# Optimization experiments

Measured on AMD Instinct MI355X. Metric: run time of the kernel, lower is better.

Reference implementation:

```python
import jax, jax.numpy as jnp
import numpy as np

# dims (see shape_source)
N = 20000      # spots / graph nodes
G = 3000       # genes
NF = 256       # NFeature = CrossAttention dim
D_IN = 256     # dims_spot[0]
HID = 64       # dims_spot[1]
OUT = 16       # dims_spot[2]
H = 3          # GATv2 heads
E1 = 640000
E2 = 320000
SLOPE = 0.2    # leaky relu negative slope (GATv2 + CrossAttention alpha)


def _gat_params(key, din, hid, heads):
    k = jax.random.split(key, 3)
    s = 1.0 / np.sqrt(din)
    Wl = jax.random.normal(k[0], (din, heads * hid), jnp.float32) * s
    Wr = jax.random.normal(k[1], (din, heads * hid), jnp.float32) * s
    att = jax.random.normal(k[2], (heads, hid), jnp.float32) * s
    bl = jnp.zeros((heads * hid,), jnp.float32)
    br = jnp.zeros((heads * hid,), jnp.float32)
    b = jnp.zeros((hid,), jnp.float32)
    return Wl, bl, Wr, br, att, b


def setup_inputs() -> dict:
    key = jax.random.key(0)
    ks = jax.random.split(key, 16)
    inp = {
        "gene_freq_mtx": jax.random.normal(ks[0], (NF, G), jnp.float32),
        "gene_eigvecs_T": jax.random.normal(ks[1], (G, N), jnp.float32) / np.sqrt(G),
        "spot_freq_mtx": jax.random.normal(ks[2], (N, D_IN), jnp.float32),
        "spot_eigvecs_T": jax.random.normal(ks[3], (D_IN, NF), jnp.float32) / np.sqrt(D_IN),
        "spotnet": jax.random.randint(ks[4], (2, E1), 0, N, jnp.int32),
        "spotnet_cluster": jax.random.randint(ks[5], (2, E2), 0, N, jnp.int32),
    }
    for name, din, kk in [("c1", D_IN, ks[6]), ("c1p", D_IN, ks[7]), ("c3", OUT, ks[8]), ("c3p", OUT, ks[9])]:
        Wl, bl, Wr, br, att, b = _gat_params(kk, din, HID, H)
        inp[name + "_Wl"] = Wl; inp[name + "_bl"] = bl
        inp[name + "_Wr"] = Wr; inp[name + "_br"] = br
        inp[name + "_att"] = att; inp[name + "_b"] = b
    inp["W2"] = jax.random.normal(ks[10], (2 * HID, OUT), jnp.float32) / np.sqrt(2 * HID)
    inp["b2"] = jnp.zeros((OUT,), jnp.float32)
    inp["W4"] = jax.random.normal(ks[11], (2 * HID, D_IN), jnp.float32) / np.sqrt(2 * HID)
    inp["b4"] = jnp.zeros((D_IN,), jnp.float32)
    inp["a1"] = jax.random.normal(ks[12], (2 * NF, 1), jnp.float32) * 0.05
    inp["a2"] = jax.random.normal(ks[13], (2 * NF, 1), jnp.float32) * 0.05
    return inp


def gatv2(x, edge_index, Wl, bl, Wr, br, att, b, n):
    """PyG GATv2Conv, concat=False (head mean), add_self_loops=False, eval mode."""
    heads, c = att.shape
    src, dst = edge_index[0], edge_index[1]
    xl = (x @ Wl + bl).reshape(-1, heads, c)   # source transform [N,H,C]
    xr = (x @ Wr + br).reshape(-1, heads, c)   # target transform [N,H,C]
    m = jax.nn.leaky_relu(xl[src] + xr[dst], SLOPE)          # [E,H,C]
    e = jnp.einsum('ehc,hc->eh', m, att)                      # [E,H]
    emax = jax.ops.segment_max(e, dst, num_segments=n)        # [N,H]
    emax = jnp.where(jnp.isfinite(emax), emax, 0.0)           # empty segments
    p = jnp.exp(e - emax[dst])
    denom = jax.ops.segment_sum(p, dst, num_segments=n)       # [N,H]
    alpha = p / jnp.maximum(denom, 1e-16)[dst]                # segment softmax
    out = jax.ops.segment_sum(alpha[:, :, None] * xl[src], dst, num_segments=n)
    return out.mean(axis=1) + b                                # [N,C]


def reference(gene_freq_mtx, gene_eigvecs_T, spot_freq_mtx, spot_eigvecs_T,
              c1_Wl, c1_bl, c1_Wr, c1_br, c1_att, c1_b,
              c1p_Wl, c1p_bl, c1p_Wr, c1p_br, c1p_att, c1p_b,
              W2, b2,
              c3_Wl, c3_bl, c3_Wr, c3_br, c3_att, c3_b,
              c3p_Wl, c3p_bl, c3p_Wr, c3p_br, c3p_att, c3p_b,
              W4, b4, a1, a2, spotnet, spotnet_cluster):
    n = spot_freq_mtx.shape[0]
    # GAT (cluster=True)
    h1n = gatv2(spot_freq_mtx, spotnet, c1_Wl, c1_bl, c1_Wr, c1_br, c1_att, c1_b, n)
    h1p = gatv2(spot_freq_mtx, spotnet_cluster, c1p_Wl, c1p_bl, c1p_Wr, c1p_br, c1p_att, c1p_b, n)
    h1 = jax.nn.elu(jnp.concatenate([h1n, h1p], axis=1))
    h2 = h1 @ W2 + b2                                          # emb_spot [N,OUT]
    h3n = gatv2(h2, spotnet, c3_Wl, c3_bl, c3_Wr, c3_br, c3_att, c3_b, n)
    h3p = gatv2(h2, spotnet_cluster, c3p_Wl, c3p_bl, c3p_Wr, c3p_br, c3p_att, c3p_b, n)
    h3 = jax.nn.elu(jnp.concatenate([h3n, h3p], axis=1))
    h4 = h3 @ W4 + b4                                          # mtx_res_spot [N,D_IN]
    # iGFT + clip-at-zero (== relu)
    Xg = jax.nn.relu(gene_eigvecs_T.T @ gene_freq_mtx.T)       # [N,NF]
    Xs = jax.nn.relu(h4 @ spot_eigvecs_T)                      # [N,NF]
    # CrossAttention (dropout=0.0)
    cat = jnp.concatenate([Xg, Xs], axis=1)                    # [N,2NF]
    e = jax.nn.leaky_relu(jnp.concatenate([cat @ a1, cat @ a2], axis=1), SLOPE)
    lam = jax.nn.softmax(e, axis=1)                            # [N,2]
    res = lam[:, :1] * Xg + lam[:, 1:] * Xs
    return (res, lam, h2, h4)
```

## Files before the change

kernel.cpp:

```cpp
#include <hip/hip_runtime.h>

typedef unsigned short u16;
typedef __attribute__((ext_vector_type(8))) short bf16x8;
typedef __attribute__((ext_vector_type(4))) float floatx4;

#define NSPOT 20000
#define NGENE 3000
#define E1N   640000
#define E2N   320000

#define OFF_RES 0
#define OFF_LAM 5120000
#define OFF_H2  5160000
#define OFF_H4  5480000

__device__ __forceinline__ float b2f(u16 u){
  union { unsigned int i; float f; } v; v.i = ((unsigned int)u) << 16; return v.f;
}
__device__ __forceinline__ u16 f2b(float f){
  union { float f; unsigned int i; } v; v.f = f;
  unsigned int i = v.i;
  return (u16)((i + 0x7FFFu + ((i >> 16) & 1u)) >> 16);
}
__device__ __forceinline__ void stout(void* O, size_t i, float v, int isbf){
  if (isbf) ((u16*)O)[i] = f2b(v); else ((float*)O)[i] = v;
}
__device__ __forceinline__ u16 ldu(const void* p, size_t i, int isbf){
  return isbf ? ((const u16*)p)[i] : f2b(((const float*)p)[i]);
}

__global__ void sniff_kernel(const u16* __restrict__ x, int* __restrict__ flag){
  int lane = threadIdx.x;
  u16 u = x[lane * 2];
  int e = (u >> 7) & 0xFF;
  int sane = (u == 0) || (e >= 0x60 && e <= 0xA0);
  unsigned long long b = __ballot(sane);
  if (lane == 0) flag[0] = (__popcll(b) >= 48) ? 1 : 0;
}

struct ConvSeg { const void* src; u16* dst; int n; };
struct ConvBatch { ConvSeg s[14]; };
__global__ void convbatch_kernel(ConvBatch cb, const int* __restrict__ dflag){
  ConvSeg S = cb.s[blockIdx.y];
  int i = blockIdx.x * 256 + threadIdx.x;
  if (i < S.n) S.dst[i] = ldu(S.src, i, dflag[0]);
}

__global__ void conv4_kernel(const void* __restrict__ src, u16* __restrict__ dst, int n4,
                             const int* __restrict__ dflag){
  int i = blockIdx.x * 256 + threadIdx.x;
  if (i >= n4) return;
  size_t b = (size_t)i * 4;
  u16 o[4];
  if (dflag[0]){
    *(uint2*)o = *(const uint2*)((const u16*)src + b);
  } else {
    float4 f = *(const float4*)((const float*)src + b);
    o[0]=f2b(f.x); o[1]=f2b(f.y); o[2]=f2b(f.z); o[3]=f2b(f.w);
  }
  *(uint2*)(dst + b) = *(uint2*)o;
}

__global__ __launch_bounds__(256) void transpose_kernel(
    const void* __restrict__ GE, u16* __restrict__ AT,
    const int* __restrict__ dflag, int K, int M){
  __shared__ float tile[64 * 65];
  int isbf = dflag[0];
  int m0 = blockIdx.x * 64, k0 = blockIdx.y * 64;
#pragma unroll
  for (int i = 0; i < 4; i++){
    int idx = threadIdx.x + i * 256;
    int kr = idx >> 4, mc = (idx & 15) * 4;
    int gk = k0 + kr, gm = m0 + mc;
    if (gk < K){
      float v0 = 0.f, v1 = 0.f, v2 = 0.f, v3 = 0.f;
      if (gm + 4 <= M){
        if (isbf){
          const u16* pp = (const u16*)GE + (size_t)gk * M + gm;
          v0 = b2f(pp[0]); v1 = b2f(pp[1]); v2 = b2f(pp[2]); v3 = b2f(pp[3]);
        } else {
          float4 f = *(const float4*)((const float*)GE + (size_t)gk * M + gm);
          v0 = f.x; v1 = f.y; v2 = f.z; v3 = f.w;
        }
      } else {
        for (int e = 0; e < 4; e++){
          if (gm + e < M){
            float t = isbf ? b2f(((const u16*)GE)[(size_t)gk * M + gm + e])
                           : ((const float*)GE)[(size_t)gk * M + gm + e];
            if (e == 0) v0 = t; else if (e == 1) v1 = t; else if (e == 2) v2 = t; else v3 = t;
          }
        }
      }
      tile[(mc + 0) * 65 + kr] = v0;
      tile[(mc + 1) * 65 + kr] = v1;
      tile[(mc + 2) * 65 + kr] = v2;
      tile[(mc + 3) * 65 + kr] = v3;
    }
  }
  __syncthreads();
#pragma unroll
  for (int i = 0; i < 2; i++){
    int idx = threadIdx.x + i * 256;
    int mr = idx >> 3, kc = (idx & 7) * 8;
    int gm = m0 + mr, gk = k0 + kc;
    if (gm < M && gk < K){
      if (gk + 8 <= K){
        u16 o[8];
#pragma unroll
        for (int e = 0; e < 8; e++) o[e] = f2b(tile[mr * 65 + kc + e]);
        *(uint4*)&AT[(size_t)gm * K + gk] = *(uint4*)o;
      } else {
        for (int e = 0; e < 8 && gk + e < K; e++)
          AT[(size_t)gm * K + gk + e] = f2b(tile[mr * 65 + kc + e]);
      }
    }
  }
}

__global__ void hist_kernel(const int* __restrict__ dst, int* __restrict__ cnt, int E){
  int e = blockIdx.x * 256 + threadIdx.x;
  if (e < E){ int d = dst[e]; if ((unsigned)d < (unsigned)NSPOT) atomicAdd(&cnt[d], 1); }
}

__global__ void scan_kernel(const int* __restrict__ cnt, int* __restrict__ off,
                            int* __restrict__ cur, int n){
  __shared__ int part[256];
  int tid = threadIdx.x;
  int chunk = (n + 255) / 256;
  int lo = tid * chunk; if (lo > n) lo = n;
  int hi = lo + chunk; if (hi > n) hi = n;
  int s = 0;
  for (int i = lo; i < hi; i++) s += cnt[i];
  part[tid] = s;
  __syncthreads();
  if (tid == 0){
    int run = 0;
    for (int i = 0; i < 256; i++){ int t = part[i]; part[i] = run; run += t; }
  }
  __syncthreads();
  int run = part[tid];
  for (int i = lo; i < hi; i++){ off[i] = run; cur[i] = run; run += cnt[i]; }
  if (hi == n) off[n] = run;
}

__global__ void scatter_kernel(const int* __restrict__ src, const int* __restrict__ dst,
                               int* __restrict__ cur, int* __restrict__ out, int E){
  int e = blockIdx.x * 256 + threadIdx.x;
  if (e < E){
    int d = dst[e];
    if ((unsigned)d < (unsigned)NSPOT){
      int p = atomicAdd(&cur[d], 1);
      if ((unsigned)p < (unsigned)E) out[p] = src[e];
    }
  }
}

__global__ void assemble_kernel(const void* Wl, const void* bl, const void* Wr, const void* br,
                                const void* Wlp, const void* blp, const void* Wrp, const void* brp,
                                u16* __restrict__ Wcat, u16* __restrict__ bcat, int Kdim,
                                const int* __restrict__ dflag){
  int isbf = dflag[0];
  int idx = blockIdx.x * 256 + threadIdx.x;
  int total = Kdim * 768;
  if (idx < total){
    int k = idx / 768, j = idx % 768;
    int seg = j / 192, jj = j % 192;
    const void* W = (seg == 0) ? Wl : (seg == 1) ? Wr : (seg == 2) ? Wlp : Wrp;
    Wcat[idx] = ldu(W, (size_t)k * 192 + jj, isbf);
  }
  if (idx < 768){
    int seg = idx / 192, jj = idx % 192;
    const void* b = (seg == 0) ? bl : (seg == 1) ? br : (seg == 2) ? blp : brp;
    bcat[idx] = ldu(b, jj, isbf);
  }
}

template<int BMI, bool A_KM, bool B_NK, bool A_EXT, bool B_EXT, bool RELU, bool HAS_BIAS, bool C_OUT>
__global__ __launch_bounds__(256) void gemm_mfma(
    const void* __restrict__ A, const void* __restrict__ B,
    const u16* __restrict__ bias, void* __restrict__ Cp,
    const int* __restrict__ dflag, size_t aoff, size_t coff,
    int M, int N, int K, int lda, int ldb, int ldc)
{
  const int isbf = dflag[0];
  constexpr int BM = 64 * BMI, BK = 32, LDA = BK + 8, LDB = BK + 8;
  __shared__ __align__(16) u16 As[BM * LDA];
  __shared__ __align__(16) u16 Bs[64 * LDB];
  const u16*   A16 = (const u16*)A + aoff;
  const float* A32 = (const float*)A + aoff;
  const u16*   B16 = (const u16*)B;
  const float* B32 = (const float*)B;
  auto ldA = [&](size_t i) -> u16 { return (!A_EXT || isbf) ? A16[i] : f2b(A32[i]); };
  auto ldB = [&](size_t i) -> u16 { return (!B_EXT || isbf) ? B16[i] : f2b(B32[i]); };

  int tid = threadIdx.x;
  int lane = tid & 63, w = tid >> 6;
  int m0 = blockIdx.y * BM, n0 = blockIdx.x * 64;
  floatx4 acc[BMI][4] = {};
  int quad = lane >> 4;
  int nk = (K + BK - 1) / BK;
  for (int kt = 0; kt < nk; kt++){
    int k0 = kt * BK;
    if (!A_KM){
#pragma unroll
      for (int i = 0; i < BMI; i++){
        int id = tid + i * 256;
        int r = id >> 2, c = (id & 3) * 8;
        int gm = m0 + r, gk = k0 + c;
        if (gm < M && gk + 8 <= K){
          if (!A_EXT || isbf){
            *(uint4*)&As[r * LDA + c] = *(const uint4*)(A16 + (size_t)gm * lda + gk);
          } else {
            const float* p = A32 + (size_t)gm * lda + gk;
            float4 f0 = *(const float4*)p, f1 = *(const float4*)(p + 4);
            u16* d = &As[r * LDA + c];
            d[0]=f2b(f0.x); d[1]=f2b(f0.y); d[2]=f2b(f0.z); d[3]=f2b(f0.w);
            d[4]=f2b(f1.x); d[5]=f2b(f1.y); d[6]=f2b(f1.z); d[7]=f2b(f1.w);
          }
        } else {
          for (int e = 0; e < 8; e++)
            As[r * LDA + c + e] = (gm < M && gk + e < K) ? ldA((size_t)gm * lda + gk + e) : (u16)0;
        }
      }
    } else {
#pragma unroll
      for (int i = 0; i < BMI; i++){
        int id = tid + i * 256;
        int kk, rr;
        if (BMI == 2){ kk = id >> 4; rr = (id & 15) * 8; }
        else         { kk = id >> 3; rr = (id & 7) * 8; }
        int gk = k0 + kk, gm = m0 + rr;
        if (gk < K && gm + 8 <= M){
          if (!A_EXT || isbf){
            uint4 v = *(const uint4*)(A16 + (size_t)gk * lda + gm);
            const u16* pv = (const u16*)&v;
#pragma unroll
            for (int e = 0; e < 8; e++) As[(rr + e) * LDA + kk] = pv[e];
          } else {
            const float* p = A32 + (size_t)gk * lda + gm;
            float4 f0 = *(const float4*)p, f1 = *(const float4*)(p + 4);
            As[(rr+0)*LDA+kk]=f2b(f0.x); As[(rr+1)*LDA+kk]=f2b(f0.y);
            As[(rr+2)*LDA+kk]=f2b(f0.z); As[(rr+3)*LDA+kk]=f2b(f0.w);
            As[(rr+4)*LDA+kk]=f2b(f1.x); As[(rr+5)*LDA+kk]=f2b(f1.y);
            As[(rr+6)*LDA+kk]=f2b(f1.z); As[(rr+7)*LDA+kk]=f2b(f1.w);
          }
        } else {
          for (int e = 0; e < 8; e++)
            As[(rr + e) * LDA + kk] = (gk < K && gm + e < M) ? ldA((size_t)gk * lda + gm + e) : (u16)0;
        }
      }
    }
    if (B_NK){
      int r = tid >> 2, c = (tid & 3) * 8;
      int gn = n0 + r, gk = k0 + c;
      if (gn < N && gk + 8 <= K){
        if (!B_EXT || isbf){
          *(uint4*)&Bs[r * LDB + c] = *(const uint4*)(B16 + (size_t)gn * ldb + gk);
        } else {
          const float* p = B32 + (size_t)gn * ldb + gk;
          float4 f0 = *(const float4*)p, f1 = *(const float4*)(p + 4);
          u16* d = &Bs[r * LDB + c];
          d[0]=f2b(f0.x); d[1]=f2b(f0.y); d[2]=f2b(f0.z); d[3]=f2b(f0.w);
          d[4]=f2b(f1.x); d[5]=f2b(f1.y); d[6]=f2b(f1.z); d[7]=f2b(f1.w);
        }
      } else {
        for (int e = 0; e < 8; e++)
          Bs[r * LDB + c + e] = (gn < N && gk + e < K) ? ldB((size_t)gn * ldb + gk + e) : (u16)0;
      }
    } else {
      int kk = tid >> 3, nn = (tid & 7) * 8;
      int gk = k0 + kk, gn = n0 + nn;
      if (gk < K && gn + 8 <= N){
        if (!B_EXT || isbf){
          uint4 v = *(const uint4*)(B16 + (size_t)gk * ldb + gn);
          const u16* pv = (const u16*)&v;
#pragma unroll
          for (int e = 0; e < 8; e++) Bs[(nn + e) * LDB + kk] = pv[e];
        } else {
          const float* p = B32 + (size_t)gk * ldb + gn;
          float4 f0 = *(const float4*)p, f1 = *(const float4*)(p + 4);
          Bs[(nn+0)*LDB+kk]=f2b(f0.x); Bs[(nn+1)*LDB+kk]=f2b(f0.y);
          Bs[(nn+2)*LDB+kk]=f2b(f0.z); Bs[(nn+3)*LDB+kk]=f2b(f0.w);
          Bs[(nn+4)*LDB+kk]=f2b(f1.x); Bs[(nn+5)*LDB+kk]=f2b(f1.y);
          Bs[(nn+6)*LDB+kk]=f2b(f1.z); Bs[(nn+7)*LDB+kk]=f2b(f1.w);
        }
      } else {
        for (int e = 0; e < 8; e++)
          Bs[(nn + e) * LDB + kk] = (gk < K && gn + e < N) ? ldB((size_t)gk * ldb + gn + e) : (u16)0;
      }
    }
    __syncthreads();
    bf16x8 af[BMI];
#pragma unroll
    for (int mi = 0; mi < BMI; mi++)
      af[mi] = *(const bf16x8*)&As[(w * (16 * BMI) + mi * 16 + (lane & 15)) * LDA + quad * 8];
#pragma unroll
    for (int ni = 0; ni < 4; ni++){
      bf16x8 bfr = *(const bf16x8*)&Bs[(ni * 16 + (lane & 15)) * LDB + quad * 8];
#pragma unroll
      for (int mi = 0; mi < BMI; mi++)
        acc[mi][ni] = __builtin_amdgcn_mfma_f32_16x16x32_bf16(af[mi], bfr, acc[mi][ni], 0, 0, 0);
    }
    __syncthreads();
  }
#pragma unroll
  for (int mi = 0; mi < BMI; mi++)
#pragma unroll
    for (int ni = 0; ni < 4; ni++)
#pragma unroll
      for (int r = 0; r < 4; r++){
        int row = m0 + w * (16 * BMI) + mi * 16 + quad * 4 + r;
        int col = n0 + ni * 16 + (lane & 15);
        if (row < M && col < N){
          float v = acc[mi][ni][r];
          if (HAS_BIAS) v += b2f(bias[col]);
          if (RELU) v = fmaxf(v, 0.f);
          size_t ci = coff + (size_t)row * ldc + col;
          if (!C_OUT) ((u16*)Cp)[ci] = f2b(v);
          else stout(Cp, ci, v, isbf);
        }
      }
}

__global__ __launch_bounds__(256) void gat_kernel(
    const u16* __restrict__ Y, int xl_off, int xr_off,
    const int* __restrict__ off, const int* __restrict__ srcs,
    const u16* __restrict__ att, const u16* __restrict__ bias,
    u16* __restrict__ aggout, int out_off, int n, int E)
{
  int wid = (blockIdx.x * 256 + threadIdx.x) >> 6;
  int lane = threadIdx.x & 63;
  if (wid >= n) return;
  int sub = lane >> 4;
  int cbase = (lane & 15) * 4;
  const int ldY = 768;
  size_t drow = (size_t)wid * ldY;

  float xr[3][4], at[3][4];
#pragma unroll
  for (int h = 0; h < 3; h++){
    uint2 vx = *(const uint2*)(Y + drow + xr_off + h * 64 + cbase);
    uint2 va = *(const uint2*)(att + h * 64 + cbase);
    const u16* px = (const u16*)&vx;
    const u16* pa = (const u16*)&va;
#pragma unroll
    for (int j = 0; j < 4; j++){ xr[h][j] = b2f(px[j]); at[h][j] = b2f(pa[j]); }
  }

  int beg = off[wid], end = off[wid + 1];
  beg = max(0, min(beg, E));
  end = max(beg, min(end, E));

  float mh[3] = {-INFINITY, -INFINITY, -INFINITY};
  float lh[3] = {0.f, 0.f, 0.f};
  float ac[3][4] = {};

  uint2 xa[3] = {};
  int s_b = 0;
  if (beg < end){
    int e0 = beg + sub;
    int s = (e0 < end) ? srcs[e0] : 0;
    if ((unsigned)s >= (unsigned)NSPOT) s = 0;
    const u16* p = Y + (size_t)s * ldY + xl_off + cbase;
#pragma unroll
    for (int h = 0; h < 3; h++) xa[h] = *(const uint2*)(p + h * 64);
    if (beg + 4 < end){
      int e1 = beg + 4 + sub;
      int s1 = (e1 < end) ? srcs[e1] : 0;
      if ((unsigned)s1 >= (unsigned)NSPOT) s1 = 0;
      s_b = s1;
    }
  }

  for (int b = beg; b < end; b += 4){
    uint2 xc[3];
#pragma unroll
    for (int h = 0; h < 3; h++) xc[h] = xa[h];
    bool act = (b + sub) < end;

    if (b + 4 < end){
      const u16* p = Y + (size_t)s_b * ldY + xl_off + cbase;
#pragma unroll
      for (int h = 0; h < 3; h++) xa[h] = *(const uint2*)(p + h * 64);
      if (b + 8 < end){
        int e2 = b + 8 + sub;
        int s2 = (e2 < end) ? srcs[e2] : 0;
        if ((unsigned)s2 >= (unsigned)NSPOT) s2 = 0;
        s_b = s2;
      }
    }

    float xl[3][4];
    float t0, t1, t2;
    {
      float a0 = 0.f, a1 = 0.f, a2 = 0.f;
      const u16* p0 = (const u16*)&xc[0];
      const u16* p1 = (const u16*)&xc[1];
      const u16* p2 = (const u16*)&xc[2];
#pragma unroll
      for (int j = 0; j < 4; j++){
        float x0 = b2f(p0[j]); xl[0][j] = x0;
        float u0 = x0 + xr[0][j]; u0 = fmaxf(u0, 0.2f * u0);
        a0 = __builtin_fmaf(at[0][j], u0, a0);
        float x1 = b2f(p1[j]); xl[1][j] = x1;
        float u1 = x1 + xr[1][j]; u1 = fmaxf(u1, 0.2f * u1);
        a1 = __builtin_fmaf(at[1][j], u1, a1);
        float x2 = b2f(p2[j]); xl[2][j] = x2;
        float u2 = x2 + xr[2][j]; u2 = fmaxf(u2, 0.2f * u2);
        a2 = __builtin_fmaf(at[2][j], u2, a2);
      }
      t0 = a0; t1 = a1; t2 = a2;
    }
#pragma unroll
    for (int d = 1; d < 16; d <<= 1){
      t0 += __shfl_xor(t0, d, 64);
      t1 += __shfl_xor(t1, d, 64);
      t2 += __shfl_xor(t2, d, 64);
    }
    if (act){
      float tt[3] = {t0, t1, t2};
#pragma unroll
      for (int h = 0; h < 3; h++){
        float nm = fmaxf(mh[h], tt[h]);
        if (nm > mh[h]){
          float sc = __expf(mh[h] - nm);
          lh[h] *= sc;
#pragma unroll
          for (int j = 0; j < 4; j++) ac[h][j] *= sc;
          mh[h] = nm;
        }
        float w = __expf(tt[h] - mh[h]);
        lh[h] += w;
#pragma unroll
        for (int j = 0; j < 4; j++) ac[h][j] = __builtin_fmaf(w, xl[h][j], ac[h][j]);
      }
    }
  }

  float o[4] = {0.f, 0.f, 0.f, 0.f};
#pragma unroll
  for (int h = 0; h < 3; h++){
    float gm = fmaxf(mh[h], __shfl_xor(mh[h], 16, 64));
    gm = fmaxf(gm, __shfl_xor(gm, 32, 64));
    float sc = (mh[h] == -INFINITY) ? 0.f : __expf(mh[h] - gm);
    float L = lh[h] * sc;
    L += __shfl_xor(L, 16, 64);
    L += __shfl_xor(L, 32, 64);
    float inv = 1.f / fmaxf(L, 1e-16f);
#pragma unroll
    for (int j = 0; j < 4; j++){
      float a = ac[h][j] * sc;
      a += __shfl_xor(a, 16, 64);
      a += __shfl_xor(a, 32, 64);
      o[j] += a * inv;
    }
  }
  if (sub == 0){
    u16 ov[4];
#pragma unroll
    for (int j = 0; j < 4; j++){
      float v = o[j] * (1.f / 3.f) + b2f(bias[cbase + j]);
      v = (v > 0.f) ? v : expm1f(v);
      if (!(fabsf(v) < 1e30f)) v = 0.f;
      ov[j] = f2b(v);
    }
    *(uint2*)&aggout[(size_t)wid * 128 + out_off + cbase] = *(uint2*)ov;
  }
}

__global__ __launch_bounds__(256) void h2_kernel(const u16* __restrict__ AGG,
                                                 const u16* __restrict__ W2, const u16* __restrict__ b2,
                                                 float* __restrict__ H2, void* __restrict__ OUT,
                                                 const int* __restrict__ dflag, int n){
  __shared__ float w2s[128 * 16];
  __shared__ float as_[16][128];
  int isbf = dflag[0];
  int tid = threadIdx.x;
  for (int i = tid; i < 128 * 16; i += 256) w2s[i] = b2f(W2[i]);
  int m0 = blockIdx.x * 16;
  for (int i = tid; i < 16 * 128; i += 256){
    int r = i >> 7, c = i & 127; int m = m0 + r;
    as_[r][c] = (m < n) ? b2f(AGG[(size_t)m * 128 + c]) : 0.f;
  }
  __syncthreads();
  int r = tid >> 4, j = tid & 15;
  int m = m0 + r;
  float acc = b2f(b2[j]);
  for (int k = 0; k < 128; k++) acc += as_[r][k] * w2s[k * 16 + j];
  if (m < n){
    H2[(size_t)m * 16 + j] = acc;
    stout(OUT, (size_t)OFF_H2 + (size_t)m * 16 + j, acc, isbf);
  }
}

__global__ __launch_bounds__(256) void y2_kernel(const float* __restrict__ H2,
                                                 const u16* __restrict__ Wcat2, const u16* __restrict__ bcat2,
                                                 u16* __restrict__ Y2, int n){
  __shared__ u16 ws_[16 * 768];
  __shared__ float h[16][16];
  int tid = threadIdx.x;
  for (int i = tid; i < 16 * 768; i += 256) ws_[i] = Wcat2[i];
  int m0 = blockIdx.x * 16;
  {
    int r = tid >> 4, k = tid & 15; int m = m0 + r;
    h[r][k] = (m < n) ? H2[(size_t)m * 16 + k] : 0.f;
  }
  __syncthreads();
  int j = tid;
  float acc[16][3];
  float bj0 = b2f(bcat2[j]), bj1 = b2f(bcat2[j + 256]), bj2 = b2f(bcat2[j + 512]);
#pragma unroll
  for (int r = 0; r < 16; r++){ acc[r][0] = bj0; acc[r][1] = bj1; acc[r][2] = bj2; }
  for (int k = 0; k < 16; k++){
    float w0 = b2f(ws_[k * 768 + j]);
    float w1 = b2f(ws_[k * 768 + j + 256]);
    float w2 = b2f(ws_[k * 768 + j + 512]);
#pragma unroll
    for (int r = 0; r < 16; r++){
      float hv = h[r][k];
      acc[r][0] += hv * w0; acc[r][1] += hv * w1; acc[r][2] += hv * w2;
    }
  }
#pragma unroll
  for (int r = 0; r < 16; r++){
    int m = m0 + r;
    if (m < n){
      size_t base = (size_t)m * 768;
      Y2[base + j] = f2b(acc[r][0]);
      Y2[base + j + 256] = f2b(acc[r][1]);
      Y2[base + j + 512] = f2b(acc[r][2]);
    }
  }
}

__global__ __launch_bounds__(256) void cross_attn_kernel(
    const u16* __restrict__ XG, const u16* __restrict__ XS,
    const u16* __restrict__ a1, const u16* __restrict__ a2,
    void* __restrict__ OUT, const int* __restrict__ dflag, int n){
  int wid = (blockIdx.x * 256 + threadIdx.x) >> 6;
  int lane = threadIdx.x & 63;
  if (wid >= n) return;
  int isbf = dflag[0];
  int c0 = lane * 4;
  size_t base = (size_t)wid * 256 + c0;
  float g[4], s[4];
#pragma unroll
  for (int e = 0; e < 4; e++){ g[e] = b2f(XG[base + e]); s[e] = b2f(XS[base + e]); }
  float p1 = 0.f, p2 = 0.f;
#pragma unroll
  for (int e = 0; e < 4; e++){
    p1 += g[e] * b2f(a1[c0 + e]) + s[e] * b2f(a1[256 + c0 + e]);
    p2 += g[e] * b2f(a2[c0 + e]) + s[e] * b2f(a2[256 + c0 + e]);
  }
#pragma unroll
  for (int d = 32; d > 0; d >>= 1){
    p1 += __shfl_xor(p1, d, 64);
    p2 += __shfl_xor(p2, d, 64);
  }
  float e1 = (p1 > 0.f) ? p1 : 0.2f * p1;
  float e2 = (p2 > 0.f) ? p2 : 0.2f * p2;
  float mx = fmaxf(e1, e2);
  float w1 = __expf(e1 - mx), w2 = __expf(e2 - mx);
  float inv = 1.f / (w1 + w2);
  float l0 = w1 * inv, l1 = w2 * inv;
#pragma unroll
  for (int e = 0; e < 4; e++)
    stout(OUT, (size_t)OFF_RES + base + e, l0 * g[e] + l1 * s[e], isbf);
  if (lane == 0){
    stout(OUT, (size_t)OFF_LAM + (size_t)wid * 2,     l0, isbf);
    stout(OUT, (size_t)OFF_LAM + (size_t)wid * 2 + 1, l1, isbf);
  }
}

extern "C" void kernel_launch(void* const* d_in, const int* in_sizes, int n_in,
                              void* d_out, int out_size, void* d_ws, size_t ws_size,
                              hipStream_t stream) {
  const void* gene_freq = d_in[0];
  const void* gene_eig  = d_in[1];
  const void* spot_freq = d_in[2];
  const void* spot_eig  = d_in[3];
  const int* net1 = (const int*)d_in[4];
  const int* net2 = (const int*)d_in[5];
  const void *c1_Wl=d_in[6],  *c1_bl=d_in[7],  *c1_Wr=d_in[8],  *c1_br=d_in[9],  *c1_att=d_in[10], *c1_b=d_in[11];
  const void *c1p_Wl=d_in[12],*c1p_bl=d_in[13],*c1p_Wr=d_in[14],*c1p_br=d_in[15],*c1p_att=d_in[16],*c1p_b=d_in[17];
  const void *c3_Wl=d_in[18], *c3_bl=d_in[19], *c3_Wr=d_in[20], *c3_br=d_in[21], *c3_att=d_in[22], *c3_b=d_in[23];
  const void *c3p_Wl=d_in[24],*c3p_bl=d_in[25],*c3p_Wr=d_in[26],*c3p_br=d_in[27],*c3p_att=d_in[28],*c3p_b=d_in[29];
  const void *W2=d_in[30], *b2=d_in[31], *W4=d_in[32], *b4=d_in[33], *a1=d_in[34], *a2=d_in[35];

  char* p0 = (char*)d_ws;
  char* p = p0;
  auto carve = [&](size_t bytes) -> char* {
    char* r = p; p += (bytes + 255) & ~(size_t)255; return r;
  };
  int*   flag  = (int*) carve(256);
  int*   cnt1  = (int*) carve((NSPOT + 2) * 4);
  int*   off1  = (int*) carve((NSPOT + 2) * 4);
  int*   cur1  = (int*) carve((NSPOT + 2) * 4);
  int*   srcs1 = (int*) carve((size_t)E1N * 4);
  int*   cnt2  = (int*) carve((NSPOT + 2) * 4);
  int*   off2  = (int*) carve((NSPOT + 2) * 4);
  int*   cur2  = (int*) carve((NSPOT + 2) * 4);
  int*   srcs2 = (int*) carve((size_t)E2N * 4);
  u16*   Wcat1 = (u16*) carve(256 * 768 * 2);
  u16*   bcat1 = (u16*) carve(2048);
  u16*   Wcat2 = (u16*) carve(16 * 768 * 2);
  u16*   bcat2 = (u16*) carve(2048);
  u16*   attc1  = (u16*)carve(192 * 2);
  u16*   attc1p = (u16*)carve(192 * 2);
  u16*   attc3  = (u16*)carve(192 * 2);
  u16*   attc3p = (u16*)carve(192 * 2);
  u16*   bc1  = (u16*)carve(64 * 2);
  u16*   bc1p = (u16*)carve(64 * 2);
  u16*   bc3  = (u16*)carve(64 * 2);
  u16*   bc3p = (u16*)carve(64 * 2);
  u16*   W2c  = (u16*)carve(2048 * 2);
  u16*   b2c  = (u16*)carve(16 * 2);
  u16*   W4c  = (u16*)carve(32768 * 2);
  u16*   b4c  = (u16*)carve(256 * 2);
  u16*   a1c  = (u16*)carve(512 * 2);
  u16*   a2c  = (u16*)carve(512 * 2);
  u16*   GF16 = (u16*) carve((size_t)256 * 3000 * 2);
  u16*   SE16 = (u16*) carve((size_t)256 * 256 * 2);
  float* H2   = (float*)carve((size_t)NSPOT * 16 * 4);
  u16*   AGG  = (u16*)  carve((size_t)NSPOT * 128 * 2);
  u16*   XGp  = (u16*)  carve((size_t)NSPOT * 256 * 2);
  char*  R    = carve(0);
  size_t used_common = (size_t)(R - p0);
  size_t needA = used_common + (size_t)NSPOT * NGENE * 2 + 4096;
  bool planA = (ws_size >= needA);

  sniff_kernel<<<1, 64, 0, stream>>>((const u16*)spot_freq, flag);
  hipMemsetAsync(cnt1, 0, NSPOT * 4, stream);
  hipMemsetAsync(cnt2, 0, NSPOT * 4, stream);
  hist_kernel<<<(E1N + 255) / 256, 256, 0, stream>>>(net1 + E1N, cnt1, E1N);
  hist_kernel<<<(E2N + 255) / 256, 256, 0, stream>>>(net2 + E2N, cnt2, E2N);
  scan_kernel<<<1, 256, 0, stream>>>(cnt1, off1, cur1, NSPOT);
  scan_kernel<<<1, 256, 0, stream>>>(cnt2, off2, cur2, NSPOT);
  scatter_kernel<<<(E1N + 255) / 256, 256, 0, stream>>>(net1, net1 + E1N, cur1, srcs1, E1N);
  scatter_kernel<<<(E2N + 255) / 256, 256, 0, stream>>>(net2, net2 + E2N, cur2, srcs2, E2N);

  ConvBatch cb;
  cb.s[0]  = {c1_att,  attc1,  192}; cb.s[1]  = {c1p_att, attc1p, 192};
  cb.s[2]  = {c3_att,  attc3,  192}; cb.s[3]  = {c3p_att, attc3p, 192};
  cb.s[4]  = {c1_b, bc1, 64}; cb.s[5]  = {c1p_b, bc1p, 64};
  cb.s[6]  = {c3_b, bc3, 64}; cb.s[7]  = {c3p_b, bc3p, 64};
  cb.s[8]  = {W2, W2c, 2048}; cb.s[9]  = {b2, b2c, 16};
  cb.s[10] = {W4, W4c, 32768}; cb.s[11] = {b4, b4c, 256};
  cb.s[12] = {a1, a1c, 512}; cb.s[13] = {a2, a2c, 512};
  convbatch_kernel<<<dim3(128, 14), 256, 0, stream>>>(cb, flag);
  conv4_kernel<<<(256 * 3000 / 4 + 255) / 256, 256, 0, stream>>>(gene_freq, GF16, 256 * 3000 / 4, flag);
  conv4_kernel<<<(256 * 256 / 4 + 255) / 256, 256, 0, stream>>>(spot_eig, SE16, 256 * 256 / 4, flag);

  assemble_kernel<<<(256 * 768 + 255) / 256, 256, 0, stream>>>(
      c1_Wl, c1_bl, c1_Wr, c1_br, c1p_Wl, c1p_bl, c1p_Wr, c1p_br, Wcat1, bcat1, 256, flag);
  assemble_kernel<<<(16 * 768 + 255) / 256, 256, 0, stream>>>(
      c3_Wl, c3_bl, c3_Wr, c3_br, c3p_Wl, c3p_bl, c3p_Wr, c3p_br, Wcat2, bcat2, 16, flag);

  if (planA){
    u16* AT   = (u16*)R;
    u16* SF16 = (u16*)R;
    u16* Y    = (u16*)(R + 10485760);
    u16* XS   = (u16*)(R + 10485760 + 31457280);
    u16* XG   = XGp;

    transpose_kernel<<<dim3(313, 47), 256, 0, stream>>>(gene_eig, AT, flag, NGENE, NSPOT);
    gemm_mfma<1, false, true, false, false, true, false, false><<<dim3(4, 313), 256, 0, stream>>>(
        AT, GF16, nullptr, XG, flag, 0, 0, NSPOT, 256, NGENE, NGENE, NGENE, 256);
    conv4_kernel<<<(NSPOT * 256 / 4 + 255) / 256, 256, 0, stream>>>(spot_freq, SF16, NSPOT * 256 / 4, flag);
    gemm_mfma<2, false, false, false, false, false, true, false><<<dim3(12, 157), 256, 0, stream>>>(
        SF16, Wcat1, bcat1, Y, flag, 0, 0, NSPOT, 768, 256, 256, 768, 768);
    gat_kernel<<<5000, 256, 0, stream>>>(Y, 0,   192, off1, srcs1, attc1,  bc1,  AGG, 0,  NSPOT, E1N);
    gat_kernel<<<5000, 256, 0, stream>>>(Y, 384, 576, off2, srcs2, attc1p, bc1p, AGG, 64, NSPOT, E2N);
    h2_kernel<<<1250, 256, 0, stream>>>(AGG, W2c, b2c, H2, d_out, flag, NSPOT);
    y2_kernel<<<1250, 256, 0, stream>>>(H2, Wcat2, bcat2, Y, NSPOT);
    gat_kernel<<<5000, 256, 0, stream>>>(Y, 0,   192, off1, srcs1, attc3,  bc3,  AGG, 0,  NSPOT, E1N);
    gat_kernel<<<5000, 256, 0, stream>>>(Y, 384, 576, off2, srcs2, attc3p, bc3p, AGG, 64, NSPOT, E2N);
    gemm_mfma<1, false, false, false, false, false, true, true><<<dim3(4, 313), 256, 0, stream>>>(
        AGG, W4c, b4c, d_out, flag, 0, OFF_H4, NSPOT, 256, 128, 128, 256, 256);
    gemm_mfma<1, false, false, true, false, true, false, false><<<dim3(4, 313), 256, 0, stream>>>(
        d_out, SE16, nullptr, XS, flag, OFF_H4, 0, NSPOT, 256, 256, 256, 256, 256);
    cross_attn_kernel<<<5000, 256, 0, stream>>>(XG, XS, a1c, a2c, d_out, flag, NSPOT);
  } else {
    u16* Y  = (u16*)R;
    u16* XG = Y;
    u16* XS = Y + 5120000;
    gemm_mfma<2, false, false, true, false, false, true, false><<<dim3(12, 157), 256, 0, stream>>>(
        spot_freq, Wcat1, bcat1, Y, flag, 0, 0, NSPOT, 768, 256, 256, 768, 768);
    gat_kernel<<<5000, 256, 0, stream>>>(Y, 0,   192, off1, srcs1, attc1,  bc1,  AGG, 0,  NSPOT, E1N);
    gat_kernel<<<5000, 256, 0, stream>>>(Y, 384, 576, off2, srcs2, attc1p, bc1p, AGG, 64, NSPOT, E2N);
    h2_kernel<<<1250, 256, 0, stream>>>(AGG, W2c, b2c, H2, d_out, flag, NSPOT);
    y2_kernel<<<1250, 256, 0, stream>>>(H2, Wcat2, bcat2, Y, NSPOT);
    gat_kernel<<<5000, 256, 0, stream>>>(Y, 0,   192, off1, srcs1, attc3,  bc3,  AGG, 0,  NSPOT, E1N);
    gat_kernel<<<5000, 256, 0, stream>>>(Y, 384, 576, off2, srcs2, attc3p, bc3p, AGG, 64, NSPOT, E2N);
    gemm_mfma<2, false, false, false, false, false, true, true><<<dim3(4, 157), 256, 0, stream>>>(
        AGG, W4c, b4c, d_out, flag, 0, OFF_H4, NSPOT, 256, 128, 128, 256, 256);
    gemm_mfma<2, false, false, true, true, true, false, false><<<dim3(4, 157), 256, 0, stream>>>(
        d_out, spot_eig, nullptr, XS, flag, OFF_H4, 0, NSPOT, 256, 256, 256, 256, 256);
    gemm_mfma<2, true, true, true, true, true, false, false><<<dim3(4, 157), 256, 0, stream>>>(
        gene_eig, gene_freq, nullptr, XG, flag, 0, 0, NSPOT, 256, NGENE, NSPOT, NGENE, 256);
    cross_attn_kernel<<<5000, 256, 0, stream>>>(XG, XS, a1c, a2c, d_out, flag, NSPOT);
  }

  (void)in_sizes; (void)n_in; (void)out_size; (void)ws_size;
}
```

Measured before the change: 1.122 ms.

## Batch paired launches, fuse h2/y2, add bf16 h4 side output, enlarge GEMM tiles

After: 1.091 ms. 1.03x faster.

```diff
diff --git a/kernel.cpp b/kernel.cpp
--- a/kernel.cpp
+++ b/kernel.cpp
@@ -46,11 +46,17 @@
   if (i < S.n) S.dst[i] = ldu(S.src, i, dflag[0]);
 }
 
-__global__ void conv4_kernel(const void* __restrict__ src, u16* __restrict__ dst, int n4,
+__global__ void conv3_kernel(const void* __restrict__ s0, u16* __restrict__ d0, int n0,
+                             const void* __restrict__ s1, u16* __restrict__ d1, int n1,
+                             const void* __restrict__ s2, u16* __restrict__ d2, int n2,
                              const int* __restrict__ dflag){
   int i = blockIdx.x * 256 + threadIdx.x;
-  if (i >= n4) return;
-  size_t b = (size_t)i * 4;
+  const void* src; u16* dst; int local;
+  if (i < n0){ src = s0; dst = d0; local = i; }
+  else if (i < n0 + n1){ src = s1; dst = d1; local = i - n0; }
+  else if (i < n0 + n1 + n2){ src = s2; dst = d2; local = i - n0 - n1; }
+  else return;
+  size_t b = (size_t)local * 4;
   u16 o[4];
   if (dflag[0]){
     *(uint2*)o = *(const uint2*)((const u16*)src + b);
@@ -117,13 +123,21 @@
   }
 }
 
-__global__ void hist_kernel(const int* __restrict__ dst, int* __restrict__ cnt, int E){
+__global__ void hist2_kernel(const int* __restrict__ dst0, int E0, int* __restrict__ cnt0,
+                             const int* __restrict__ dst1, int E1, int* __restrict__ cnt1){
+  const int* dst = blockIdx.y ? dst1 : dst0;
+  int* cnt = blockIdx.y ? cnt1 : cnt0;
+  int E = blockIdx.y ? E1 : E0;
   int e = blockIdx.x * 256 + threadIdx.x;
   if (e < E){ int d = dst[e]; if ((unsigned)d < (unsigned)NSPOT) atomicAdd(&cnt[d], 1); }
 }
 
-__global__ void scan_kernel(const int* __restrict__ cnt, int* __restrict__ off,
-                            int* __restrict__ cur, int n){
+__global__ void scan2_kernel(const int* __restrict__ c0, int* __restrict__ o0, int* __restrict__ u0,
+                             const int* __restrict__ c1, int* __restrict__ o1, int* __restrict__ u1,
+                             int n){
+  const int* cnt = blockIdx.x ? c1 : c0;
+  int* off = blockIdx.x ? o1 : o0;
+  int* cur = blockIdx.x ? u1 : u0;
   __shared__ int part[256];
   int tid = threadIdx.x;
   int chunk = (n + 255) / 256;
@@ -143,8 +157,15 @@
   if (hi == n) off[n] = run;
 }
 
-__global__ void scatter_kernel(const int* __restrict__ src, const int* __restrict__ dst,
-                               int* __restrict__ cur, int* __restrict__ out, int E){
+__global__ void scatter2_kernel(const int* __restrict__ src0, const int* __restrict__ dst0,
+                                int* __restrict__ cur0, int* __restrict__ out0, int E0,
+                                const int* __restrict__ src1, const int* __restrict__ dst1,
+                                int* __restrict__ cur1, int* __restrict__ out1, int E1){
+  const int* src = blockIdx.y ? src1 : src0;
+  const int* dst = blockIdx.y ? dst1 : dst0;
+  int* cur = blockIdx.y ? cur1 : cur0;
+  int* out = blockIdx.y ? out1 : out0;
+  int E = blockIdx.y ? E1 : E0;
   int e = blockIdx.x * 256 + threadIdx.x;
   if (e < E){
     int d = dst[e];
@@ -155,32 +176,34 @@
   }
 }
 
-__global__ void assemble_kernel(const void* Wl, const void* bl, const void* Wr, const void* br,
-                                const void* Wlp, const void* blp, const void* Wrp, const void* brp,
-                                u16* __restrict__ Wcat, u16* __restrict__ bcat, int Kdim,
-                                const int* __restrict__ dflag){
+struct AsmSet {
+  const void *Wl, *bl, *Wr, *br, *Wlp, *blp, *Wrp, *brp;
+  u16* Wcat; u16* bcat; int Kdim;
+};
+__global__ void assemble2_kernel(AsmSet s0, AsmSet s1, const int* __restrict__ dflag){
+  AsmSet S = blockIdx.y ? s1 : s0;
   int isbf = dflag[0];
   int idx = blockIdx.x * 256 + threadIdx.x;
-  int total = Kdim * 768;
+  int total = S.Kdim * 768;
   if (idx < total){
     int k = idx / 768, j = idx % 768;
     int seg = j / 192, jj = j % 192;
-    const void* W = (seg == 0) ? Wl : (seg == 1) ? Wr : (seg == 2) ? Wlp : Wrp;
-    Wcat[idx] = ldu(W, (size_t)k * 192 + jj, isbf);
+    const void* W = (seg == 0) ? S.Wl : (seg == 1) ? S.Wr : (seg == 2) ? S.Wlp : S.Wrp;
+    S.Wcat[idx] = ldu(W, (size_t)k * 192 + jj, isbf);
   }
   if (idx < 768){
     int seg = idx / 192, jj = idx % 192;
-    const void* b = (seg == 0) ? bl : (seg == 1) ? br : (seg == 2) ? blp : brp;
-    bcat[idx] = ldu(b, jj, isbf);
-  }
-}
-
-template<int BMI, bool A_KM, bool B_NK, bool A_EXT, bool B_EXT, bool RELU, bool HAS_BIAS, bool C_OUT>
+    const void* b = (seg == 0) ? S.bl : (seg == 1) ? S.br : (seg == 2) ? S.blp : S.brp;
+    S.bcat[idx] = ldu(b, jj, isbf);
+  }
+}
+
+template<int BMI, bool A_KM, bool B_NK, bool A_EXT, bool B_EXT, bool RELU, bool HAS_BIAS, bool C_OUT, bool C2>
 __global__ __launch_bounds__(256) void gemm_mfma(
     const void* __restrict__ A, const void* __restrict__ B,
-    const u16* __restrict__ bias, void* __restrict__ Cp,
+    const u16* __restrict__ bias, void* __restrict__ Cp, u16* __restrict__ Cp2,
     const int* __restrict__ dflag, size_t aoff, size_t coff,
-    int M, int N, int K, int lda, int ldb, int ldc)
+    int M, int N, int K, int lda, int ldb, int ldc, int ldc2)
 {
   const int isbf = dflag[0];
   constexpr int BM = 64 * BMI, BK = 32, LDA = BK + 8, LDB = BK + 8;
@@ -318,17 +341,24 @@
           size_t ci = coff + (size_t)row * ldc + col;
           if (!C_OUT) ((u16*)Cp)[ci] = f2b(v);
           else stout(Cp, ci, v, isbf);
+          if (C2) Cp2[(size_t)row * ldc2 + col] = f2b(v);
         }
       }
 }
 
-__global__ __launch_bounds__(256) void gat_kernel(
-    const u16* __restrict__ Y, int xl_off, int xr_off,
-    const int* __restrict__ off, const int* __restrict__ srcs,
-    const u16* __restrict__ att, const u16* __restrict__ bias,
-    u16* __restrict__ aggout, int out_off, int n, int E)
+struct GatSet {
+  const int* off; const int* srcs; const u16* att; const u16* bias;
+  int xl_off, xr_off, out_off, E;
+};
+__global__ __launch_bounds__(256) void gat2_kernel(
+    const u16* __restrict__ Y, GatSet SA, GatSet SB,
+    u16* __restrict__ aggout, int n)
 {
-  int wid = (blockIdx.x * 256 + threadIdx.x) >> 6;
+  int half = gridDim.x >> 1;
+  int selB = (int)blockIdx.x >= half;
+  GatSet S = selB ? SB : SA;
+  int bx = blockIdx.x - (selB ? half : 0);
+  int wid = (bx * 256 + threadIdx.x) >> 6;
   int lane = threadIdx.x & 63;
   if (wid >= n) return;
   int sub = lane >> 4;
@@ -339,17 +369,17 @@
   float xr[3][4], at[3][4];
 #pragma unroll
   for (int h = 0; h < 3; h++){
-    uint2 vx = *(const uint2*)(Y + drow + xr_off + h * 64 + cbase);
-    uint2 va = *(const uint2*)(att + h * 64 + cbase);
+    uint2 vx = *(const uint2*)(Y + drow + S.xr_off + h * 64 + cbase);
+    uint2 va = *(const uint2*)(S.att + h * 64 + cbase);
     const u16* px = (const u16*)&vx;
     const u16* pa = (const u16*)&va;
 #pragma unroll
     for (int j = 0; j < 4; j++){ xr[h][j] = b2f(px[j]); at[h][j] = b2f(pa[j]); }
   }
 
-  int beg = off[wid], end = off[wid + 1];
-  beg = max(0, min(beg, E));
-  end = max(beg, min(end, E));
+  int beg = S.off[wid], end = S.off[wid + 1];
+  beg = max(0, min(beg, S.E));
+  end = max(beg, min(end, S.E));
 
   float mh[3] = {-INFINITY, -INFINITY, -INFINITY};
   float lh[3] = {0.f, 0.f, 0.f};
@@ -359,14 +389,14 @@
   int s_b = 0;
   if (beg < end){
     int e0 = beg + sub;
-    int s = (e0 < end) ? srcs[e0] : 0;
+    int s = (e0 < end) ? S.srcs[e0] : 0;
     if ((unsigned)s >= (unsigned)NSPOT) s = 0;
-    const u16* p = Y + (size_t)s * ldY + xl_off + cbase;
+    const u16* p = Y + (size_t)s * ldY + S.xl_off + cbase;
 #pragma unroll
     for (int h = 0; h < 3; h++) xa[h] = *(const uint2*)(p + h * 64);
     if (beg + 4 < end){
       int e1 = beg + 4 + sub;
-      int s1 = (e1 < end) ? srcs[e1] : 0;
+      int s1 = (e1 < end) ? S.srcs[e1] : 0;
       if ((unsigned)s1 >= (unsigned)NSPOT) s1 = 0;
       s_b = s1;
     }
@@ -379,12 +409,12 @@
     bool act = (b + sub) < end;
 
     if (b + 4 < end){
-      const u16* p = Y + (size_t)s_b * ldY + xl_off + cbase;
+      const u16* p = Y + (size_t)s_b * ldY + S.xl_off + cbase;
 #pragma unroll
       for (int h = 0; h < 3; h++) xa[h] = *(const uint2*)(p + h * 64);
       if (b + 8 < end){
         int e2 = b + 8 + sub;
-        int s2 = (e2 < end) ? srcs[e2] : 0;
+        int s2 = (e2 < end) ? S.srcs[e2] : 0;
         if ((unsigned)s2 >= (unsigned)NSPOT) s2 = 0;
         s_b = s2;
       }
@@ -459,51 +489,41 @@
     u16 ov[4];
 #pragma unroll
     for (int j = 0; j < 4; j++){
-      float v = o[j] * (1.f / 3.f) + b2f(bias[cbase + j]);
+      float v = o[j] * (1.f / 3.f) + b2f(S.bias[cbase + j]);
       v = (v > 0.f) ? v : expm1f(v);
       if (!(fabsf(v) < 1e30f)) v = 0.f;
       ov[j] = f2b(v);
     }
-    *(uint2*)&aggout[(size_t)wid * 128 + out_off + cbase] = *(uint2*)ov;
-  }
-}
-
-__global__ __launch_bounds__(256) void h2_kernel(const u16* __restrict__ AGG,
-                                                 const u16* __restrict__ W2, const u16* __restrict__ b2,
-                                                 float* __restrict__ H2, void* __restrict__ OUT,
-                                                 const int* __restrict__ dflag, int n){
+    *(uint2*)&aggout[(size_t)wid * 128 + S.out_off + cbase] = *(uint2*)ov;
+  }
+}
+
+__global__ __launch_bounds__(256) void h2y2_kernel(
+    const u16* __restrict__ AGG, const u16* __restrict__ W2, const u16* __restrict__ b2,
+    const u16* __restrict__ Wcat2, const u16* __restrict__ bcat2,
+    void* __restrict__ OUT, u16* __restrict__ Y2,
+    const int* __restrict__ dflag, int n){
   __shared__ float w2s[128 * 16];
   __shared__ float as_[16][128];
+  __shared__ float h[16][16];
+  __shared__ __align__(16) u16 ws_[16 * 768];
   int isbf = dflag[0];
   int tid = threadIdx.x;
   for (int i = tid; i < 128 * 16; i += 256) w2s[i] = b2f(W2[i]);
+  for (int i = tid; i < 1536; i += 256) ((uint4*)ws_)[i] = ((const uint4*)Wcat2)[i];
   int m0 = blockIdx.x * 16;
   for (int i = tid; i < 16 * 128; i += 256){
     int r = i >> 7, c = i & 127; int m = m0 + r;
     as_[r][c] = (m < n) ? b2f(AGG[(size_t)m * 128 + c]) : 0.f;
   }
   __syncthreads();
-  int r = tid >> 4, j = tid & 15;
-  int m = m0 + r;
-  float acc = b2f(b2[j]);
-  for (int k = 0; k < 128; k++) acc += as_[r][k] * w2s[k * 16 + j];
-  if (m < n){
-    H2[(size_t)m * 16 + j] = acc;
-    stout(OUT, (size_t)OFF_H2 + (size_t)m * 16 + j, acc, isbf);
-  }
-}
-
-__global__ __launch_bounds__(256) void y2_kernel(const float* __restrict__ H2,
-                                                 const u16* __restrict__ Wcat2, const u16* __restrict__ bcat2,
-                                                 u16* __restrict__ Y2, int n){
-  __shared__ u16 ws_[16 * 768];
-  __shared__ float h[16][16];
-  int tid = threadIdx.x;
-  for (int i = tid; i < 16 * 768; i += 256) ws_[i] = Wcat2[i];
-  int m0 = blockIdx.x * 16;
   {
-    int r = tid >> 4, k = tid & 15; int m = m0 + r;
-    h[r][k] = (m < n) ? H2[(size_t)m * 16 + k] : 0.f;
+    int r = tid >> 4, j = tid & 15;
+    int m = m0 + r;
+    float acc = b2f(b2[j]);
+    for (int k = 0; k < 128; k++) acc += as_[r][k] * w2s[k * 16 + j];
+    h[r][j] = acc;
+    if (m < n) stout(OUT, (size_t)OFF_H2 + (size_t)m * 16 + j, acc, isbf);
   }
   __syncthreads();
   int j = tid;
@@ -621,23 +641,26 @@
   u16*   a2c  = (u16*)carve(512 * 2);
   u16*   GF16 = (u16*) carve((size_t)256 * 3000 * 2);
   u16*   SE16 = (u16*) carve((size_t)256 * 256 * 2);
-  float* H2   = (float*)carve((size_t)NSPOT * 16 * 4);
-  u16*   AGG  = (u16*)  carve((size_t)NSPOT * 128 * 2);
-  u16*   XGp  = (u16*)  carve((size_t)NSPOT * 256 * 2);
+  u16*   SF16 = (u16*) carve((size_t)NSPOT * 256 * 2);
+  u16*   H4B  = (u16*) carve((size_t)NSPOT * 256 * 2);
+  u16*   AGG  = (u16*) carve((size_t)NSPOT * 128 * 2);
+  u16*   XGp  = (u16*) carve((size_t)NSPOT * 256 * 2);
   char*  R    = carve(0);
   size_t used_common = (size_t)(R - p0);
-  size_t needA = used_common + (size_t)NSPOT * NGENE * 2 + 4096;
+  size_t needA = used_common + (size_t)NSPOT * NGENE * 2
+               + (size_t)NSPOT * 768 * 2
+               + (size_t)NSPOT * 256 * 2
+               + 4096;
   bool planA = (ws_size >= needA);
 
   sniff_kernel<<<1, 64, 0, stream>>>((const u16*)spot_freq, flag);
   hipMemsetAsync(cnt1, 0, NSPOT * 4, stream);
   hipMemsetAsync(cnt2, 0, NSPOT * 4, stream);
-  hist_kernel<<<(E1N + 255) / 256, 256, 0, stream>>>(net1 + E1N, cnt1, E1N);
-  hist_kernel<<<(E2N + 255) / 256, 256, 0, stream>>>(net2 + E2N, cnt2, E2N);
-  scan_kernel<<<1, 256, 0, stream>>>(cnt1, off1, cur1, NSPOT);
-  scan_kernel<<<1, 256, 0, stream>>>(cnt2, off2, cur2, NSPOT);
-  scatter_kernel<<<(E1N + 255) / 256, 256, 0, stream>>>(net1, net1 + E1N, cur1, srcs1, E1N);
-  scatter_kernel<<<(E2N + 255) / 256, 256, 0, stream>>>(net2, net2 + E2N, cur2, srcs2, E2N);
+  hist2_kernel<<<dim3((E1N + 255) / 256, 2), 256, 0, stream>>>(
+      net1 + E1N, E1N, cnt1, net2 + E2N, E2N, cnt2);
+  scan2_kernel<<<2, 256, 0, stream>>>(cnt1, off1, cur1, cnt2, off2, cur2, NSPOT);
+  scatter2_kernel<<<dim3((E1N + 255) / 256, 2), 256, 0, stream>>>(
+      net1, net1 + E1N, cur1, srcs1, E1N, net2, net2 + E2N, cur2, srcs2, E2N);
 
   ConvBatch cb;
   cb.s[0]  = {c1_att,  attc1,  192}; cb.s[1]  = {c1p_att, attc1p, 192};
@@ -648,58 +671,51 @@
   cb.s[10] = {W4, W4c, 32768}; cb.s[11] = {b4, b4c, 256};
   cb.s[12] = {a1, a1c, 512}; cb.s[13] = {a2, a2c, 512};
   convbatch_kernel<<<dim3(128, 14), 256, 0, stream>>>(cb, flag);
-  conv4_kernel<<<(256 * 3000 / 4 + 255) / 256, 256, 0, stream>>>(gene_freq, GF16, 256 * 3000 / 4, flag);
-  conv4_kernel<<<(256 * 256 / 4 + 255) / 256, 256, 0, stream>>>(spot_eig, SE16, 256 * 256 / 4, flag);
-
-  assemble_kernel<<<(256 * 768 + 255) / 256, 256, 0, stream>>>(
-      c1_Wl, c1_bl, c1_Wr, c1_br, c1p_Wl, c1p_bl, c1p_Wr, c1p_br, Wcat1, bcat1, 256, flag);
-  assemble_kernel<<<(16 * 768 + 255) / 256, 256, 0, stream>>>(
-      c3_Wl, c3_bl, c3_Wr, c3_br, c3p_Wl, c3p_bl, c3p_Wr, c3p_br, Wcat2, bcat2, 16, flag);
-
+
+  {
+    int n0 = 256 * 3000 / 4, n1 = 256 * 256 / 4, n2 = NSPOT * 256 / 4;
+    int tot = n0 + n1 + n2;
+    conv3_kernel<<<(tot + 255) / 256, 256, 0, stream>>>(
+        gene_freq, GF16, n0, spot_eig, SE16, n1, spot_freq, SF16, n2, flag);
+  }
+
+  AsmSet as0 = {c1_Wl, c1_bl, c1_Wr, c1_br, c1p_Wl, c1p_bl, c1p_Wr, c1p_br, Wcat1, bcat1, 256};
+  AsmSet as1 = {c3_Wl, c3_bl, c3_Wr, c3_br, c3p_Wl, c3p_bl, c3p_Wr, c3p_br, Wcat2, bcat2, 16};
+  assemble2_kernel<<<dim3((256 * 768 + 255) / 256, 2), 256, 0, stream>>>(as0, as1, flag);
+
+  GatSet g1a = {off1, srcs1, attc1,  bc1,  0,   192, 0,  E1N};
+  GatSet g1b = {off2, srcs2, attc1p, bc1p, 384, 576, 64, E2N};
+  GatSet g3a = {off1, srcs1, attc3,  bc3,  0,   192, 0,  E1N};
+  GatSet g3b = {off2, srcs2, attc3p, bc3p, 384, 576, 64, E2N};
+
+  u16* Y;
+  u16* XS;
+  u16* XG = XGp;
   if (planA){
-    u16* AT   = (u16*)R;
-    u16* SF16 = (u16*)R;
-    u16* Y    = (u16*)(R + 10485760);
-    u16* XS   = (u16*)(R + 10485760 + 31457280);
-    u16* XG   = XGp;
+    u16* AT = (u16*)R;
+    Y  = (u16*)(R + (size_t)NSPOT * NGENE * 2);
+    XS = Y + (size_t)NSPOT * 768;
 
     transpose_kernel<<<dim3(313, 47), 256, 0, stream>>>(gene_eig, AT, flag, NGENE, NSPOT);
-    gemm_mfma<1, false, true, false, false, true, false, false><<<dim3(4, 313), 256, 0, stream>>>(
-        AT, GF16, nullptr, XG, flag, 0, 0, NSPOT, 256, NGENE, NGENE, NGENE, 256);
-    conv4_kernel<<<(NSPOT * 256 / 4 + 255) / 256, 256, 0, stream>>>(spot_freq, SF16, NSPOT * 256 / 4, flag);
-    gemm_mfma<2, false, false, false, false, false, true, false><<<dim3(12, 157), 256, 0, stream>>>(
-        SF16, Wcat1, bcat1, Y, flag, 0, 0, NSPOT, 768, 256, 256, 768, 768);
-    gat_kernel<<<5000, 256, 0, stream>>>(Y, 0,   192, off1, srcs1, attc1,  bc1,  AGG, 0,  NSPOT, E1N);
-    gat_kernel<<<5000, 256, 0, stream>>>(Y, 384, 576, off2, srcs2, attc1p, bc1p, AGG, 64, NSPOT, E2N);
-    h2_kernel<<<1250, 256, 0, stream>>>(AGG, W2c, b2c, H2, d_out, flag, NSPOT);
-    y2_kernel<<<1250, 256, 0, stream>>>(H2, Wcat2, bcat2, Y, NSPOT);
-    gat_kernel<<<5000, 256, 0, stream>>>(Y, 0,   192, off1, srcs1, attc3,  bc3,  AGG, 0,  NSPOT, E1N);
-    gat_kernel<<<5000, 256, 0, stream>>>(Y, 384, 576, off2, srcs2, attc3p, bc3p, AGG, 64, NSPOT, E2N);
-    gemm_mfma<1, false, false, false, false, false, true, true><<<dim3(4, 313), 256, 0, stream>>>(
-        AGG, W4c, b4c, d_out, flag, 0, OFF_H4, NSPOT, 256, 128, 128, 256, 256);
-    gemm_mfma<1, false, false, true, false, true, false, false><<<dim3(4, 313), 256, 0, stream>>>(
-        d_out, SE16, nullptr, XS, flag, OFF_H4, 0, NSPOT, 256, 256, 256, 256, 256);
-    cross_attn_kernel<<<5000, 256, 0, stream>>>(XG, XS, a1c, a2c, d_out, flag, NSPOT);
+    gemm_mfma<2, false, true, false, false, true, false, false, false><<<dim3(4, 157), 256, 0, stream>>>(
+        AT, GF16, nullptr, XG, nullptr, flag, 0, 0, NSPOT, 256, NGENE, NGENE, NGENE, 256, 0);
   } else {
-    u16* Y  = (u16*)R;
-    u16* XG = Y;
-    u16* XS = Y + 5120000;
-    gemm_mfma<2, false, false, true, false, false, true, false><<<dim3(12, 157), 256, 0, stream>>>(
-        spot_freq, Wcat1, bcat1, Y, flag, 0, 0, NSPOT, 768, 256, 256, 768, 768);
-    gat_kernel<<<5000, 256, 0, stream>>>(Y, 0,   192, off1, srcs1, attc1,  bc1,  AGG, 0,  NSPOT, E1N);
-    gat_kernel<<<5000, 256, 0, stream>>>(Y, 384, 576, off2, srcs2, attc1p, bc1p, AGG, 64, NSPOT, E2N);
-    h2_kernel<<<1250, 256, 0, stream>>>(AGG, W2c, b2c, H2, d_out, flag, NSPOT);
-    y2_kernel<<<1250, 256, 0, stream>>>(H2, Wcat2, bcat2, Y, NSPOT);
-    gat_kernel<<<5000, 256, 0, stream>>>(Y, 0,   192, off1, srcs1, attc3,  bc3,  AGG, 0,  NSPOT, E1N);
-    gat_kernel<<<5000, 256, 0, stream>>>(Y, 384, 576, off2, srcs2, attc3p, bc3p, AGG, 64, NSPOT, E2N);
-    gemm_mfma<2, false, false, false, false, false, true, true><<<dim3(4, 157), 256, 0, stream>>>(
-        AGG, W4c, b4c, d_out, flag, 0, OFF_H4, NSPOT, 256, 128, 128, 256, 256);
-    gemm_mfma<2, false, false, true, true, true, false, false><<<dim3(4, 157), 256, 0, stream>>>(
-        d_out, spot_eig, nullptr, XS, flag, OFF_H4, 0, NSPOT, 256, 256, 256, 256, 256);
-    gemm_mfma<2, true, true, true, true, true, false, false><<<dim3(4, 157), 256, 0, stream>>>(
-        gene_eig, gene_freq, nullptr, XG, flag, 0, 0, NSPOT, 256, NGENE, NSPOT, NGENE, 256);
-    cross_attn_kernel<<<5000, 256, 0, stream>>>(XG, XS, a1c, a2c, d_out, flag, NSPOT);
-  }
+    Y  = (u16*)R;
+    XS = Y + (size_t)NSPOT * 768;
+    gemm_mfma<2, true, true, true, true, true, false, false, false><<<dim3(4, 157), 256, 0, stream>>>(
+        gene_eig, gene_freq, nullptr, XG, nullptr, flag, 0, 0, NSPOT, 256, NGENE, NSPOT, NGENE, 256, 0);
+  }
+
+  gemm_mfma<2, false, false, false, false, false, true, false, false><<<dim3(12, 157), 256, 0, stream>>>(
+      SF16, Wcat1, bcat1, Y, nullptr, flag, 0, 0, NSPOT, 768, 256, 256, 768, 768, 0);
+  gat2_kernel<<<10000, 256, 0, stream>>>(Y, g1a, g1b, AGG, NSPOT);
+  h2y2_kernel<<<1250, 256, 0, stream>>>(AGG, W2c, b2c, Wcat2, bcat2, d_out, Y, flag, NSPOT);
+  gat2_kernel<<<10000, 256, 0, stream>>>(Y, g3a, g3b, AGG, NSPOT);
+  gemm_mfma<2, false, false, false, false, false, true, true, true><<<dim3(4, 157), 256, 0, stream>>>(
+      AGG, W4c, b4c, d_out, H4B, flag, 0, OFF_H4, NSPOT, 256, 128, 128, 256, 256, 256);
+  gemm_mfma<2, false, false, false, false, true, false, false, false><<<dim3(4, 157), 256, 0, stream>>>(
+      H4B, SE16, nullptr, XS, nullptr, flag, 0, 0, NSPOT, 256, 256, 256, 256, 256, 0);
+  cross_attn_kernel<<<5000, 256, 0, stream>>>(XG, XS, a1c, a2c, d_out, flag, NSPOT);
 
   (void)in_sizes; (void)n_in; (void)out_size; (void)ws_size;
 }
```
